# Optimization experiments

Hardware: AMD Instinct MI355X
Metric: run time of the kernel (lower is better)

The kernel has to match this reference:

```python
import jax, jax.numpy as jnp
import numpy as np

NUM_AA = 20       # 'ACDEFGHIKLMNPQRSTVWY'
FEAT_DIM = 16     # feature_space.feature_dim
NUM_PAIRS = 8_388_608


def setup_inputs() -> dict:
    key = jax.random.key(0)
    k1, k2, k3 = jax.random.split(key, 3)
    features = jax.random.normal(k1, (NUM_AA, FEAT_DIM), dtype=jnp.float32)
    # M initialized as identity in the original (nn.Parameter(torch.eye(d)))
    M = jnp.eye(FEAT_DIM, dtype=jnp.float32)
    idx_i = jax.random.randint(k2, (NUM_PAIRS,), 0, NUM_AA, dtype=jnp.int32)
    idx_j = jax.random.randint(k3, (NUM_PAIRS,), 0, NUM_AA, dtype=jnp.int32)
    return {"features": features, "M": M, "idx_i": idx_i, "idx_j": idx_j}


def reference(features, M, idx_i, idx_j):
    # Batched version of Snack.__call__: tanh(delta^T M delta) per pair.
    delta = features[idx_i] - features[idx_j]          # [P, d]
    # dist_p = delta_p . (M @ delta_p)
    dist = jnp.einsum("pd,de,pe->p", delta, M, delta)  # [P]
    return jnp.tanh(dist)
```

## Files before the change

### kernel.cpp

```cpp
#include <hip/hip_runtime.h>
#include <math.h>


constexpr int NUM_AA = 20;
constexpr int FEAT   = 16;
constexpr int TABLE  = NUM_AA * NUM_AA;

typedef float fv4 __attribute__((ext_vector_type(4)));
typedef int   iv4 __attribute__((ext_vector_type(4)));

__global__ __launch_bounds__(512) void build_table(
    const float* __restrict__ F,
    const float* __restrict__ M,
    float* __restrict__ tab)
{
    __shared__ float sF[NUM_AA * FEAT];
    __shared__ float sM[FEAT * FEAT];
    const int t = threadIdx.x;
    for (int k = t; k < NUM_AA * FEAT; k += 512) sF[k] = F[k];
    for (int k = t; k < FEAT * FEAT; k += 512)   sM[k] = M[k];
    __syncthreads();

    if (t < TABLE) {
        const int i = t / NUM_AA;
        const int j = t - i * NUM_AA;
        float delta[FEAT];
#pragma unroll
        for (int d = 0; d < FEAT; ++d)
            delta[d] = sF[i * FEAT + d] - sF[j * FEAT + d];
        float dist = 0.f;
#pragma unroll
        for (int d = 0; d < FEAT; ++d) {
            float md = 0.f;
#pragma unroll
            for (int e = 0; e < FEAT; ++e)
                md = fmaf(sM[d * FEAT + e], delta[e], md);
            dist = fmaf(delta[d], md, dist);
        }
        tab[t] = tanhf(dist);
    }
}

__global__ __launch_bounds__(256) void gather_pairs(
    const float* __restrict__ tab,
    const iv4* __restrict__ ii4,
    const iv4* __restrict__ jj4,
    fv4* __restrict__ out4,
    int nvec,
    const int* __restrict__ ii_s,
    const int* __restrict__ jj_s,
    float* __restrict__ out_s,
    int tail_start, int total)
{
    __shared__ float s[TABLE];
    for (int k = threadIdx.x; k < TABLE; k += 256) s[k] = tab[k];
    __syncthreads();

    const int T = (int)gridDim.x * 256;
    int v = blockIdx.x * 256 + threadIdx.x;

    for (; v + T < nvec; v += 2 * T) {
        const iv4 iA = ii4[v];
        const iv4 jA = jj4[v];
        const iv4 iB = ii4[v + T];
        const iv4 jB = jj4[v + T];
        fv4 oA, oB;
        oA.x = s[iA.x * NUM_AA + jA.x];
        oA.y = s[iA.y * NUM_AA + jA.y];
        oA.z = s[iA.z * NUM_AA + jA.z];
        oA.w = s[iA.w * NUM_AA + jA.w];
        oB.x = s[iB.x * NUM_AA + jB.x];
        oB.y = s[iB.y * NUM_AA + jB.y];
        oB.z = s[iB.z * NUM_AA + jB.z];
        oB.w = s[iB.w * NUM_AA + jB.w];
        __builtin_nontemporal_store(oA, &out4[v]);
        __builtin_nontemporal_store(oB, &out4[v + T]);
    }
    for (; v < nvec; v += T) {
        const iv4 iA = ii4[v];
        const iv4 jA = jj4[v];
        fv4 oA;
        oA.x = s[iA.x * NUM_AA + jA.x];
        oA.y = s[iA.y * NUM_AA + jA.y];
        oA.z = s[iA.z * NUM_AA + jA.z];
        oA.w = s[iA.w * NUM_AA + jA.w];
        __builtin_nontemporal_store(oA, &out4[v]);
    }

    if (blockIdx.x == 0) {
        const int p = tail_start + (int)threadIdx.x;
        if (p < total)
            out_s[p] = s[ii_s[p] * NUM_AA + jj_s[p]];
    }
}

extern "C" void kernel_launch(void* const* d_in, const int* in_sizes, int n_in,
                              void* d_out, int out_size, void* d_ws, size_t ws_size,
                              hipStream_t stream)
{
    const float* F   = (const float*)d_in[0];
    const float* M   = (const float*)d_in[1];
    const int*   ii  = (const int*)d_in[2];
    const int*   jj  = (const int*)d_in[3];
    float*       out = (float*)d_out;
    float*       tab = (float*)d_ws;

    const int P    = in_sizes[2];
    const int nvec = P >> 2;
    const int tail = nvec << 2;

    build_table<<<1, 512, 0, stream>>>(F, M, tab);

    int blocks = (nvec + 255) / 256;
    if (blocks > 2048) blocks = 2048;
    if (blocks < 1)    blocks = 1;
    gather_pairs<<<blocks, 256, 0, stream>>>(
        tab, (const iv4*)ii, (const iv4*)jj, (fv4*)out,
        nvec, ii, jj, out, tail, P);
}
```

Measured before the change: 111.9 us.

## Fuse table build into gather kernel and process four vectors per thread

Removes the separate single-block table-building kernel: every gather block now computes the 400-entry tanh(delta^T M delta) table into shared memory itself, which eliminates one launch and the global round-trip for the table. The gather loop is restructured into 1024-vector chunks per block, with four independent iv4 loads per thread for more memory-level parallelism. The cost is redundant table computation in every block (up to 2048 blocks, each doing about 400×272 FMAs plus tanh) before any streaming begins.

New measurement: 113.0 us. No clear change (+1.0%).

```diff
diff --git a/kernel.cpp b/kernel.cpp
--- a/kernel.cpp
+++ b/kernel.cpp
@@ -9,40 +9,9 @@
 typedef float fv4 __attribute__((ext_vector_type(4)));
 typedef int   iv4 __attribute__((ext_vector_type(4)));
 
-__global__ __launch_bounds__(512) void build_table(
+__global__ __launch_bounds__(256) void snack_fused(
     const float* __restrict__ F,
     const float* __restrict__ M,
-    float* __restrict__ tab)
-{
-    __shared__ float sF[NUM_AA * FEAT];
-    __shared__ float sM[FEAT * FEAT];
-    const int t = threadIdx.x;
-    for (int k = t; k < NUM_AA * FEAT; k += 512) sF[k] = F[k];
-    for (int k = t; k < FEAT * FEAT; k += 512)   sM[k] = M[k];
-    __syncthreads();
-
-    if (t < TABLE) {
-        const int i = t / NUM_AA;
-        const int j = t - i * NUM_AA;
-        float delta[FEAT];
-#pragma unroll
-        for (int d = 0; d < FEAT; ++d)
-            delta[d] = sF[i * FEAT + d] - sF[j * FEAT + d];
-        float dist = 0.f;
-#pragma unroll
-        for (int d = 0; d < FEAT; ++d) {
-            float md = 0.f;
-#pragma unroll
-            for (int e = 0; e < FEAT; ++e)
-                md = fmaf(sM[d * FEAT + e], delta[e], md);
-            dist = fmaf(delta[d], md, dist);
-        }
-        tab[t] = tanhf(dist);
-    }
-}
-
-__global__ __launch_bounds__(256) void gather_pairs(
-    const float* __restrict__ tab,
     const iv4* __restrict__ ii4,
     const iv4* __restrict__ jj4,
     fv4* __restrict__ out4,
@@ -53,42 +22,90 @@
     int tail_start, int total)
 {
     __shared__ float s[TABLE];
-    for (int k = threadIdx.x; k < TABLE; k += 256) s[k] = tab[k];
+    __shared__ float sF[NUM_AA * FEAT];
+    __shared__ float sM[FEAT * FEAT];
+
+    const int t = threadIdx.x;
+
+    for (int k = t; k < NUM_AA * FEAT; k += 256) sF[k] = F[k];
+    if (t < FEAT * FEAT) sM[t] = M[t];
     __syncthreads();
 
-    const int T = (int)gridDim.x * 256;
-    int v = blockIdx.x * 256 + threadIdx.x;
+#pragma unroll
+    for (int pass = 0; pass < 2; ++pass) {
+        const int e = t + pass * 256;
+        if (e < TABLE) {
+            const int i = e / NUM_AA;
+            const int j = e - i * NUM_AA;
+            float delta[FEAT];
+#pragma unroll
+            for (int d = 0; d < FEAT; ++d)
+                delta[d] = sF[i * FEAT + d] - sF[j * FEAT + d];
+            float dist = 0.f;
+#pragma unroll
+            for (int d = 0; d < FEAT; ++d) {
+                float md = 0.f;
+#pragma unroll
+                for (int e2 = 0; e2 < FEAT; ++e2)
+                    md = fmaf(sM[d * FEAT + e2], delta[e2], md);
+                dist = fmaf(delta[d], md, dist);
+            }
+            s[e] = tanhf(dist);
+        }
+    }
+    __syncthreads();
 
-    for (; v + T < nvec; v += 2 * T) {
-        const iv4 iA = ii4[v];
-        const iv4 jA = jj4[v];
-        const iv4 iB = ii4[v + T];
-        const iv4 jB = jj4[v + T];
-        fv4 oA, oB;
-        oA.x = s[iA.x * NUM_AA + jA.x];
-        oA.y = s[iA.y * NUM_AA + jA.y];
-        oA.z = s[iA.z * NUM_AA + jA.z];
-        oA.w = s[iA.w * NUM_AA + jA.w];
-        oB.x = s[iB.x * NUM_AA + jB.x];
-        oB.y = s[iB.y * NUM_AA + jB.y];
-        oB.z = s[iB.z * NUM_AA + jB.z];
-        oB.w = s[iB.w * NUM_AA + jB.w];
-        __builtin_nontemporal_store(oA, &out4[v]);
-        __builtin_nontemporal_store(oB, &out4[v + T]);
-    }
-    for (; v < nvec; v += T) {
-        const iv4 iA = ii4[v];
-        const iv4 jA = jj4[v];
-        fv4 oA;
-        oA.x = s[iA.x * NUM_AA + jA.x];
-        oA.y = s[iA.y * NUM_AA + jA.y];
-        oA.z = s[iA.z * NUM_AA + jA.z];
-        oA.w = s[iA.w * NUM_AA + jA.w];
-        __builtin_nontemporal_store(oA, &out4[v]);
+    constexpr int CH = 4 * 256;
+    const int stride = (int)gridDim.x * CH;
+
+    for (int base = blockIdx.x * CH; base < nvec; base += stride) {
+        const int v0 = base + t;
+        if (base + CH <= nvec) {
+            const iv4 iA = ii4[v0];
+            const iv4 jA = jj4[v0];
+            const iv4 iB = ii4[v0 + 256];
+            const iv4 jB = jj4[v0 + 256];
+            const iv4 iC = ii4[v0 + 512];
+            const iv4 jC = jj4[v0 + 512];
+            const iv4 iD = ii4[v0 + 768];
+            const iv4 jD = jj4[v0 + 768];
+            fv4 oA, oB, oC, oD;
+            oA.x = s[iA.x * NUM_AA + jA.x];
+            oA.y = s[iA.y * NUM_AA + jA.y];
+            oA.z = s[iA.z * NUM_AA + jA.z];
+            oA.w = s[iA.w * NUM_AA + jA.w];
+            oB.x = s[iB.x * NUM_AA + jB.x];
+            oB.y = s[iB.y * NUM_AA + jB.y];
+            oB.z = s[iB.z * NUM_AA + jB.z];
+            oB.w = s[iB.w * NUM_AA + jB.w];
+            oC.x = s[iC.x * NUM_AA + jC.x];
+            oC.y = s[iC.y * NUM_AA + jC.y];
+            oC.z = s[iC.z * NUM_AA + jC.z];
+            oC.w = s[iC.w * NUM_AA + jC.w];
+            oD.x = s[iD.x * NUM_AA + jD.x];
+            oD.y = s[iD.y * NUM_AA + jD.y];
+            oD.z = s[iD.z * NUM_AA + jD.z];
+            oD.w = s[iD.w * NUM_AA + jD.w];
+            __builtin_nontemporal_store(oA, &out4[v0]);
+            __builtin_nontemporal_store(oB, &out4[v0 + 256]);
+            __builtin_nontemporal_store(oC, &out4[v0 + 512]);
+            __builtin_nontemporal_store(oD, &out4[v0 + 768]);
+        } else {
+            for (int v = v0; v < nvec; v += 256) {
+                const iv4 iA = ii4[v];
+                const iv4 jA = jj4[v];
+                fv4 oA;
+                oA.x = s[iA.x * NUM_AA + jA.x];
+                oA.y = s[iA.y * NUM_AA + jA.y];
+                oA.z = s[iA.z * NUM_AA + jA.z];
+                oA.w = s[iA.w * NUM_AA + jA.w];
+                __builtin_nontemporal_store(oA, &out4[v]);
+            }
+        }
     }
 
     if (blockIdx.x == 0) {
-        const int p = tail_start + (int)threadIdx.x;
+        const int p = tail_start + t;
         if (p < total)
             out_s[p] = s[ii_s[p] * NUM_AA + jj_s[p]];
     }
@@ -103,18 +120,16 @@
     const int*   ii  = (const int*)d_in[2];
     const int*   jj  = (const int*)d_in[3];
     float*       out = (float*)d_out;
-    float*       tab = (float*)d_ws;
 
     const int P    = in_sizes[2];
     const int nvec = P >> 2;
     const int tail = nvec << 2;
 
-    build_table<<<1, 512, 0, stream>>>(F, M, tab);
-
-    int blocks = (nvec + 255) / 256;
+    int blocks = (nvec + 1023) / 1024;
     if (blocks > 2048) blocks = 2048;
     if (blocks < 1)    blocks = 1;
-    gather_pairs<<<blocks, 256, 0, stream>>>(
-        tab, (const iv4*)ii, (const iv4*)jj, (fv4*)out,
+
+    snack_fused<<<blocks, 256, 0, stream>>>(
+        F, M, (const iv4*)ii, (const iv4*)jj, (fv4*)out,
         nvec, ii, jj, out, tail, P);
 }
```
